# Kernel optimization log

Measured on AMD Instinct MI355X. Metric: run time of the kernel, lower is better.

The kernel has to match this reference:

```python
import jax, jax.numpy as jnp
import numpy as np

B, N, D = 4, 2048, 1024
THRESHOLD_FACTOR = 1.25


def setup_inputs() -> dict:
    key = jax.random.key(0)
    ks = jax.random.split(key, 8)
    s = 0.02  # init scale matching torch.randn * 0.02
    return {
        "hidden_states": jax.random.normal(ks[0], (B, N, D), jnp.float32),
        "Wq": jax.random.normal(ks[1], (D, D), jnp.float32) * s,
        "bq": jnp.zeros((D,), jnp.float32),
        "Wk": jax.random.normal(ks[2], (D, D), jnp.float32) * s,
        "bk": jnp.zeros((D,), jnp.float32),
        "Wv": jax.random.normal(ks[3], (D, D), jnp.float32) * s,
        "bv": jnp.zeros((D,), jnp.float32),
        "Wo": jax.random.normal(ks[4], (D, D), jnp.float32) * s,
        "bo": jnp.zeros((D,), jnp.float32),
        "Wtq": jax.random.normal(ks[5], (2, D), jnp.float32) * s,  # nn.Linear(D, 2)
        "btq": jnp.zeros((2,), jnp.float32),
        "Wfq": jax.random.normal(ks[6], (D, 2), jnp.float32) * s,  # HebbianLinear(2, D)
        "bfq": jnp.zeros((D,), jnp.float32),
    }


def _linear(x, W, b):
    return x @ W.T + b


def reference(hidden_states, Wq, bq, Wk, bk, Wv, bv, Wo, bo, Wtq, btq, Wfq, bfq):
    d = hidden_states.shape[-1]
    q = _linear(hidden_states, Wq, bq)
    k = _linear(hidden_states, Wk, bk)
    v = _linear(hidden_states, Wv, bv)
    scores = jnp.einsum('bid,bjd->bij', q, k) / jnp.sqrt(jnp.asarray(d, scores_dtype := q.dtype))

    # PhaseAwareBinaryAttention on 2-d quantum projection
    qp = _linear(hidden_states, Wtq, btq)            # [B, N, 2]
    diff = qp[:, :, None, :] - qp[:, None, :, :]      # [B, N, N, 2]
    dist_sq = jnp.sum(diff * diff, axis=-1)           # [B, N, N]
    phase_diff = jnp.arctan2(diff[..., 1], diff[..., 0])
    forward_bias = 0.5 * (1.0 + jnp.cos(phase_diff))
    mean_dist = jnp.mean(dist_sq, axis=(-1, -2), keepdims=True)
    std_dist = jnp.std(dist_sq, axis=(-1, -2), keepdims=True, ddof=1)  # torch unbiased std
    threshold = mean_dist + THRESHOLD_FACTOR * std_dist
    n = dist_sq.shape[-1]
    causal = jnp.tril(jnp.ones((n, n), bool))
    valid = (dist_sq <= threshold) & causal[None]
    binary_attn = valid.astype(scores.dtype) * forward_bias

    masked = jnp.where(binary_attn == 0, -jnp.inf, scores)
    weights = jax.nn.softmax(masked, axis=-1)
    context = jnp.einsum('bij,bjd->bid', weights, v)
    output = _linear(context, Wo, bo)

    # F.normalize(qp, p=2, dim=-1) with eps=1e-12
    r_embed = qp / jnp.maximum(jnp.linalg.norm(qp, axis=-1, keepdims=True), 1e-12)
    quantum_output = _linear(r_embed, Wfq, bfq)
    return hidden_states + output + 0.1 * quantum_output
```

## Files before the change

### kernel.cpp

```cpp
#include <hip/hip_runtime.h>
#include <math.h>

#define N_TOK 2048
#define DIM   1024
#define BATCH 4

typedef float v4f  __attribute__((ext_vector_type(4)));
typedef __bf16 v8bf __attribute__((ext_vector_type(8)));
typedef unsigned short v8us __attribute__((ext_vector_type(8)));

static __device__ __forceinline__ unsigned short f2bf(float f) {
  unsigned int u = __float_as_uint(f);
  u += 0x7fffu + ((u >> 16) & 1u);
  return (unsigned short)(u >> 16);
}
static __device__ __forceinline__ float bf2f(unsigned short h) {
  return __uint_as_float((unsigned int)h << 16);
}

__global__ __launch_bounds__(256) void castqp_kernel(
    const float* __restrict__ hs, const float* __restrict__ Wtq,
    const float* __restrict__ btq, unsigned short* __restrict__ hs_b,
    float2* __restrict__ qp, float2* __restrict__ remb) {
  int w = threadIdx.x >> 6, lane = threadIdx.x & 63;
  int row = blockIdx.x * 4 + w;
  const float* x = hs + (size_t)row * DIM;
  unsigned short* d = hs_b + (size_t)row * DIM;
  float a0 = 0.f, a1 = 0.f;
#pragma unroll
  for (int it = 0; it < 4; ++it) {
    int base = it * 256 + lane * 4;
    float4 v = *(const float4*)(x + base);
    float4 w0 = *(const float4*)(Wtq + base);
    float4 w1 = *(const float4*)(Wtq + DIM + base);
    ushort4 pk;
    pk.x = f2bf(v.x); pk.y = f2bf(v.y); pk.z = f2bf(v.z); pk.w = f2bf(v.w);
    *(ushort4*)(d + base) = pk;
    a0 += v.x * w0.x + v.y * w0.y + v.z * w0.z + v.w * w0.w;
    a1 += v.x * w1.x + v.y * w1.y + v.z * w1.z + v.w * w1.w;
  }
  for (int o = 32; o; o >>= 1) { a0 += __shfl_xor(a0, o); a1 += __shfl_xor(a1, o); }
  if (lane == 0) {
    a0 += btq[0]; a1 += btq[1];
    qp[row] = make_float2(a0, a1);
    float nrm = fmaxf(sqrtf(a0 * a0 + a1 * a1), 1e-12f);
    remb[row] = make_float2(a0 / nrm, a1 / nrm);
  }
}

__global__ __launch_bounds__(256) void cast_w4_kernel(
    const float* __restrict__ W0, const float* __restrict__ W1,
    const float* __restrict__ W2, const float* __restrict__ W3,
    unsigned short* __restrict__ D0, unsigned short* __restrict__ D1,
    unsigned short* __restrict__ D2, unsigned short* __restrict__ D3) {
  const float* s;
  unsigned short* d;
  switch (blockIdx.y) {
    case 0: s = W0; d = D0; break;
    case 1: s = W1; d = D1; break;
    case 2: s = W2; d = D2; break;
    default: s = W3; d = D3; break;
  }
  int i = (blockIdx.x * 256 + threadIdx.x) * 4;
  float4 v = *(const float4*)(s + i);
  d[i + 0] = f2bf(v.x); d[i + 1] = f2bf(v.y);
  d[i + 2] = f2bf(v.z); d[i + 3] = f2bf(v.w);
}

__global__ __launch_bounds__(256) void moments_kernel(
    const float2* __restrict__ qp, double* __restrict__ part) {
  int b = blockIdx.y;
  int i0 = blockIdx.x * 32;
  const float2* qb = qp + ((size_t)b << 11);
  double s1 = 0.0, s2 = 0.0;
  for (int idx = threadIdx.x; idx < 32 * N_TOK; idx += 256) {
    int i = i0 + (idx >> 11), j = idx & (N_TOK - 1);
    float2 pi = qb[i], pj = qb[j];
    float dx = pi.x - pj.x, dy = pi.y - pj.y;
    float dd = __fadd_rn(__fmul_rn(dx, dx), __fmul_rn(dy, dy));
    s1 += (double)dd;
    s2 += (double)dd * (double)dd;
  }
  int lane = threadIdx.x & 63, w = threadIdx.x >> 6;
  for (int o = 32; o; o >>= 1) { s1 += __shfl_xor(s1, o); s2 += __shfl_xor(s2, o); }
  __shared__ double red[8];
  if (lane == 0) { red[w] = s1; red[4 + w] = s2; }
  __syncthreads();
  if (threadIdx.x == 0) {
    int slot = b * 64 + blockIdx.x;
    part[slot * 2 + 0] = red[0] + red[1] + red[2] + red[3];
    part[slot * 2 + 1] = red[4] + red[5] + red[6] + red[7];
  }
}

__global__ __launch_bounds__(256) void thr_kernel(
    const double* __restrict__ part, float* __restrict__ thr) {
  int b = threadIdx.x >> 6, lane = threadIdx.x & 63;
  double s1 = part[(b * 64 + lane) * 2 + 0];
  double s2 = part[(b * 64 + lane) * 2 + 1];
  for (int o = 32; o; o >>= 1) { s1 += __shfl_xor(s1, o); s2 += __shfl_xor(s2, o); }
  if (lane == 0) {
    double n2 = (double)N_TOK * (double)N_TOK;
    double mean = s1 / n2;
    double var = (s2 - n2 * mean * mean) / (n2 - 1.0);
    if (var < 0.0) var = 0.0;
    thr[b] = (float)(mean + 1.25 * sqrt(var));
  }
}

__device__ __forceinline__ void gemm_ktile_loop(
    const unsigned short* __restrict__ Ag, const unsigned short* __restrict__ Bg,
    int ldA, int ldB, int kBeg, int kEnd,
    unsigned short* As, unsigned short* Bs, v4f acc[4][4]) {
  const int tid  = threadIdx.x;
  const int lane = tid & 63;
  const int wm   = ((tid >> 6) & 1) << 6, wn = (tid >> 7) << 6;
  const int quad = lane >> 4, l16 = lane & 15;
  const int srow = tid >> 3;
  const int scol = (tid & 7) * 8;
  for (int k0 = kBeg; k0 < kEnd; k0 += 64) {
    __syncthreads();
#pragma unroll
    for (int it = 0; it < 4; ++it) {
      int row = srow + it * 32;
      const unsigned short* ga = Ag + (size_t)row * ldA + k0 + scol;
      const unsigned short* gb = Bg + (size_t)row * ldB + k0 + scol;
      unsigned short* la = As + (size_t)(it * 256 + (tid & ~63)) * 8;
      unsigned short* lb = Bs + (size_t)(it * 256 + (tid & ~63)) * 8;
      __builtin_amdgcn_global_load_lds((const __attribute__((address_space(1))) void*)ga,
                                       (__attribute__((address_space(3))) void*)la, 16, 0, 0);
      __builtin_amdgcn_global_load_lds((const __attribute__((address_space(1))) void*)gb,
                                       (__attribute__((address_space(3))) void*)lb, 16, 0, 0);
    }
    asm volatile("s_waitcnt vmcnt(0)" ::: "memory");
    __syncthreads();
#pragma unroll
    for (int kk = 0; kk < 64; kk += 32) {
      v8bf af[4], bfv[4];
#pragma unroll
      for (int i = 0; i < 4; ++i)
        af[i] = *(const v8bf*)(As + (wm + i * 16 + l16) * 64 + kk + quad * 8);
#pragma unroll
      for (int i = 0; i < 4; ++i)
        bfv[i] = *(const v8bf*)(Bs + (wn + i * 16 + l16) * 64 + kk + quad * 8);
#pragma unroll
      for (int mi = 0; mi < 4; ++mi)
#pragma unroll
        for (int ni = 0; ni < 4; ++ni)
          acc[mi][ni] = __builtin_amdgcn_mfma_f32_16x16x32_bf16(af[mi], bfv[ni], acc[mi][ni], 0, 0, 0);
    }
  }
}

__device__ __forceinline__ void ktile64_loop(
    const unsigned short* __restrict__ Ag, const unsigned short* __restrict__ Bg,
    int ldA, int ldB, int kBeg, int kEnd,
    unsigned short* As, unsigned short* Bs, v4f acc[2][4]) {
  const int tid  = threadIdx.x;
  const int lane = tid & 63;
  const int wr   = ((tid >> 6) & 1) << 5, wc = (tid >> 7) << 6;
  const int quad = lane >> 4, l16 = lane & 15;
  const int srow = tid >> 3;
  const int scol = (tid & 7) * 8;
  for (int k0 = kBeg; k0 < kEnd; k0 += 64) {
    __syncthreads();
#pragma unroll
    for (int it = 0; it < 2; ++it) {
      const unsigned short* ga = Ag + (size_t)(srow + it * 32) * ldA + k0 + scol;
      unsigned short* la = As + (size_t)(it * 256 + (tid & ~63)) * 8;
      __builtin_amdgcn_global_load_lds((const __attribute__((address_space(1))) void*)ga,
                                       (__attribute__((address_space(3))) void*)la, 16, 0, 0);
    }
#pragma unroll
    for (int it = 0; it < 4; ++it) {
      const unsigned short* gb = Bg + (size_t)(srow + it * 32) * ldB + k0 + scol;
      unsigned short* lb = Bs + (size_t)(it * 256 + (tid & ~63)) * 8;
      __builtin_amdgcn_global_load_lds((const __attribute__((address_space(1))) void*)gb,
                                       (__attribute__((address_space(3))) void*)lb, 16, 0, 0);
    }
    asm volatile("s_waitcnt vmcnt(0)" ::: "memory");
    __syncthreads();
#pragma unroll
    for (int kk = 0; kk < 64; kk += 32) {
      v8bf af[2], bfv[4];
#pragma unroll
      for (int i = 0; i < 2; ++i)
        af[i] = *(const v8bf*)(As + (wr + i * 16 + l16) * 64 + kk + quad * 8);
#pragma unroll
      for (int i = 0; i < 4; ++i)
        bfv[i] = *(const v8bf*)(Bs + (wc + i * 16 + l16) * 64 + kk + quad * 8);
#pragma unroll
      for (int mi = 0; mi < 2; ++mi)
#pragma unroll
        for (int ni = 0; ni < 4; ++ni)
          acc[mi][ni] = __builtin_amdgcn_mfma_f32_16x16x32_bf16(af[mi], bfv[ni], acc[mi][ni], 0, 0, 0);
    }
  }
}

#define PROLOG128                                                     \
  __shared__ __attribute__((aligned(16))) unsigned short smem[2][128 * 64];\
  unsigned short* As = smem[0];                                       \
  unsigned short* Bs = smem[1];                                       \
  v4f acc[4][4];                                                      \
  _Pragma("unroll") for (int i_ = 0; i_ < 4; ++i_)                    \
  _Pragma("unroll") for (int j_ = 0; j_ < 4; ++j_)                    \
      acc[i_][j_] = v4f{0.f, 0.f, 0.f, 0.f};                          \
  const int lane = threadIdx.x & 63, w = threadIdx.x >> 6;            \
  const int wm = (w & 1) << 6, wn = (w >> 1) << 6;                    \
  const int quad = lane >> 4, l16 = lane & 15;

#define PROLOG64                                                      \
  __shared__ __attribute__((aligned(16))) unsigned short As[64 * 64]; \
  __shared__ __attribute__((aligned(16))) unsigned short Bs[128 * 64];\
  v4f acc[2][4];                                                      \
  _Pragma("unroll") for (int i_ = 0; i_ < 2; ++i_)                    \
  _Pragma("unroll") for (int j_ = 0; j_ < 4; ++j_)                    \
      acc[i_][j_] = v4f{0.f, 0.f, 0.f, 0.f};                          \
  const int lane = threadIdx.x & 63, w = threadIdx.x >> 6;            \
  const int wr = (w & 1) << 5, wc = (w >> 1) << 6;                    \
  const int quad = lane >> 4, l16 = lane & 15;

__global__ __launch_bounds__(256) void gemm_qkv_fused_kernel(
    const unsigned short* __restrict__ X, const unsigned short* __restrict__ Wqkv,
    const float* __restrict__ bq, const float* __restrict__ bk,
    const float* __restrict__ bv, unsigned short* __restrict__ q_b,
    unsigned short* __restrict__ k_b, unsigned short* __restrict__ v_t) {
  PROLOG128
  int m0 = blockIdx.y * 128, n0 = blockIdx.x * 128;
  gemm_ktile_loop(X + (size_t)m0 * DIM, Wqkv + (size_t)n0 * DIM, DIM, DIM, 0, DIM, As, Bs, acc);
  int region = n0 >> 10;
  const float* bias = region == 0 ? bq : region == 1 ? bk : bv;
  int cbase = n0 & 1023;
  if (region < 2) {
    unsigned short* dst = region == 0 ? q_b : k_b;
#pragma unroll
    for (int mi = 0; mi < 4; ++mi) {
      int row0 = m0 + wm + mi * 16 + quad * 4;
#pragma unroll
      for (int ni = 0; ni < 4; ++ni) {
        int col = cbase + wn + ni * 16 + l16;
        float bcol = bias[col];
#pragma unroll
        for (int r = 0; r < 4; ++r)
          dst[(size_t)(row0 + r) * DIM + col] = f2bf(acc[mi][ni][r] + bcol);
      }
    }
  } else {
    unsigned short* T = &smem[0][0];
    __syncthreads();
#pragma unroll
    for (int mi = 0; mi < 4; ++mi) {
      int trow = wm + mi * 16 + quad * 4;
#pragma unroll
      for (int ni = 0; ni < 4; ++ni) {
        int fcol = wn + ni * 16 + l16;
        float bcol = bias[cbase + fcol];
        ushort4 pk;
        pk.x = f2bf(acc[mi][ni][0] + bcol);
        pk.y = f2bf(acc[mi][ni][1] + bcol);
        pk.z = f2bf(acc[mi][ni][2] + bcol);
        pk.w = f2bf(acc[mi][ni][3] + bcol);
        *(ushort4*)(T + fcol * 128 + trow) = pk;
      }
    }
    __syncthreads();
    int bb = m0 >> 11, tok0 = m0 & (N_TOK - 1);
    unsigned short* dstb = v_t + ((size_t)(bb << 10) + cbase) * N_TOK + tok0;
#pragma unroll
    for (int kk2 = 0; kk2 < 8; ++kk2) {
      int c = kk2 * 256 + threadIdx.x;
      int f = c >> 4, e0 = (c & 15) * 8;
      v8us v = *(const v8us*)(T + f * 128 + e0);
      *(v8us*)(dstb + (size_t)f * N_TOK + e0) = v;
    }
  }
}

static __device__ __forceinline__ int tri_cum(int T) {
  int m = T >> 1;
  return (T & 1) ? (m + 1) * (m + 1) : m * (m + 1);
}
__global__ __launch_bounds__(256) void gemm_scores_kernel(
    const unsigned short* __restrict__ q, const unsigned short* __restrict__ k,
    const float2* __restrict__ qp, const float* __restrict__ thr,
    unsigned short* __restrict__ S) {
  PROLOG64
  int b = blockIdx.y;
  int t = blockIdx.x;
  int ti = 2 * (int)sqrtf((float)t);
  if (ti > 31) ti = 31;
  while (ti < 31 && tri_cum(ti + 1) <= t) ++ti;
  while (tri_cum(ti) > t) --ti;
  int tj = t - tri_cum(ti);
  int i0 = ti * 64, j0 = tj * 128;
  const unsigned short* qb = q + (size_t)b * N_TOK * DIM;
  const unsigned short* kb = k + (size_t)b * N_TOK * DIM;
  ktile64_loop(qb + (size_t)i0 * DIM, kb + (size_t)j0 * DIM, DIM, DIM, 0, DIM, As, Bs, acc);
  float th = thr[b];
  const float2* qpb = qp + ((size_t)b << 11);
  unsigned short* Sb = S + (size_t)b * N_TOK * N_TOK;
  float2 pjv[4];
#pragma unroll
  for (int ni = 0; ni < 4; ++ni) pjv[ni] = qpb[j0 + wc + ni * 16 + l16];
#pragma unroll
  for (int mi = 0; mi < 2; ++mi) {
#pragma unroll
    for (int r = 0; r < 4; ++r) {
      int i = i0 + wr + mi * 16 + quad * 4 + r;
      float2 pi2 = qpb[i];
#pragma unroll
      for (int ni = 0; ni < 4; ++ni) {
        int j = j0 + wc + ni * 16 + l16;
        if (j <= i) {
          float dx = pi2.x - pjv[ni].x, dy = pi2.y - pjv[ni].y;
          float dd = __fadd_rn(__fmul_rn(dx, dx), __fmul_rn(dy, dy));
          bool ok = (dd <= th);
          if (ok && dx < 0.f && fabsf(dy) <= 3e-4f * (-dx)) {
            float fb = 0.5f * (1.f + cosf(atan2f(dy, dx)));
            if (fb == 0.f) ok = false;
          }
          Sb[(size_t)i * N_TOK + j] = ok ? f2bf(acc[mi][ni][r] * 0.03125f) : 0xFF80;
        }
      }
    }
  }
}

__global__ __launch_bounds__(256) void softmax_kernel(
    const unsigned short* __restrict__ S, unsigned short* __restrict__ P) {
  int row = blockIdx.x;
  int b = row >> 11, i = row & (N_TOK - 1);
  const unsigned short* s = S + ((size_t)b * N_TOK + i) * N_TOK;
  unsigned short* p = P + ((size_t)b * N_TOK + i) * N_TOK;
  int tid = threadIdx.x, lane = tid & 63, w = tid >> 6;
  int lim = i + 1;
  int tail0 = lim & ~7, ntail = lim - tail0;
  __shared__ float redmax[4], redsum[4];
  float mx = -__builtin_inff();
  for (int j = tid * 8; j + 8 <= lim; j += 2048) {
    v8us v = *(const v8us*)(s + j);
#pragma unroll
    for (int e = 0; e < 8; ++e) mx = fmaxf(mx, bf2f(v[e]));
  }
  if (tid < ntail) mx = fmaxf(mx, bf2f(s[tail0 + tid]));
  for (int o = 32; o; o >>= 1) mx = fmaxf(mx, __shfl_xor(mx, o));
  if (lane == 0) redmax[w] = mx;
  __syncthreads();
  mx = fmaxf(fmaxf(redmax[0], redmax[1]), fmaxf(redmax[2], redmax[3]));
  float sum = 0.f;
  for (int j = tid * 8; j + 8 <= lim; j += 2048) {
    v8us v = *(const v8us*)(s + j);
#pragma unroll
    for (int e = 0; e < 8; ++e) sum += __expf(bf2f(v[e]) - mx);
  }
  if (tid < ntail) sum += __expf(bf2f(s[tail0 + tid]) - mx);
  for (int o = 32; o; o >>= 1) sum += __shfl_xor(sum, o);
  if (lane == 0) redsum[w] = sum;
  __syncthreads();
  sum = redsum[0] + redsum[1] + redsum[2] + redsum[3];
  float inv = 1.f / sum;
  for (int j = tid * 8; j + 8 <= lim; j += 2048) {
    v8us v = *(const v8us*)(s + j);
    v8us o;
#pragma unroll
    for (int e = 0; e < 8; ++e) o[e] = f2bf(__expf(bf2f(v[e]) - mx) * inv);
    *(v8us*)(p + j) = o;
  }
  if (tid < ntail) p[tail0 + tid] = f2bf(__expf(bf2f(s[tail0 + tid]) - mx) * inv);
  int zs = (lim + 7) & ~7;
  if (tid < zs - lim) p[lim + tid] = 0;
  v8us zv;
#pragma unroll
  for (int e = 0; e < 8; ++e) zv[e] = 0;
  for (int j = zs + tid * 8; j < N_TOK; j += 2048) *(v8us*)(p + j) = zv;
}

__global__ __launch_bounds__(256) void gemm_pv_kernel(
    const unsigned short* __restrict__ P, const unsigned short* __restrict__ vt,
    unsigned short* __restrict__ ctx) {
  PROLOG64
  int b = blockIdx.z;
  int ti = blockIdx.y, d0 = blockIdx.x * 128;
  int i0 = ti * 64;
  const unsigned short* Pb = P + (size_t)b * N_TOK * N_TOK;
  const unsigned short* Vb = vt + (size_t)b * DIM * N_TOK;
  int kEnd = ((ti + 2) >> 1) * 128;
  ktile64_loop(Pb + (size_t)i0 * N_TOK, Vb + (size_t)d0 * N_TOK, N_TOK, N_TOK, 0, kEnd, As, Bs, acc);
#pragma unroll
  for (int mi = 0; mi < 2; ++mi) {
    int row0 = i0 + wr + mi * 16 + quad * 4;
#pragma unroll
    for (int ni = 0; ni < 4; ++ni) {
      int d = d0 + wc + ni * 16 + l16;
#pragma unroll
      for (int r = 0; r < 4; ++r)
        ctx[((size_t)b * N_TOK + row0 + r) * DIM + d] = f2bf(acc[mi][ni][r]);
    }
  }
}

__global__ __launch_bounds__(256) void gemm_out_kernel(
    const unsigned short* __restrict__ ctx, const unsigned short* __restrict__ Wob,
    const float* __restrict__ bo, const float* __restrict__ hs,
    const float2* __restrict__ remb, const float* __restrict__ Wfq,
    const float* __restrict__ bfq, float* __restrict__ out) {
  PROLOG64
  int m0 = blockIdx.y * 64, n0 = blockIdx.x * 128;
  ktile64_loop(ctx + (size_t)m0 * DIM, Wob + (size_t)n0 * DIM, DIM, DIM, 0, DIM, As, Bs, acc);
#pragma unroll
  for (int mi = 0; mi < 2; ++mi) {
    int row0 = m0 + wr + mi * 16 + quad * 4;
#pragma unroll
    for (int ni = 0; ni < 4; ++ni) {
      int col = n0 + wc + ni * 16 + l16;
      float bias2 = bo[col] + 0.1f * bfq[col];
      float wf0 = 0.1f * Wfq[col * 2 + 0], wf1 = 0.1f * Wfq[col * 2 + 1];
#pragma unroll
      for (int r = 0; r < 4; ++r) {
        int row = row0 + r;
        float2 re = remb[row];
        out[(size_t)row * DIM + col] =
            acc[mi][ni][r] + bias2 + hs[(size_t)row * DIM + col] + re.x * wf0 + re.y * wf1;
      }
    }
  }
}

extern "C" void kernel_launch(void* const* d_in, const int* in_sizes, int n_in,
                              void* d_out, int out_size, void* d_ws, size_t ws_size,
                              hipStream_t stream) {
  const float* hs  = (const float*)d_in[0];
  const float* Wq  = (const float*)d_in[1];
  const float* bq  = (const float*)d_in[2];
  const float* Wk  = (const float*)d_in[3];
  const float* bk  = (const float*)d_in[4];
  const float* Wv  = (const float*)d_in[5];
  const float* bv  = (const float*)d_in[6];
  const float* Wo  = (const float*)d_in[7];
  const float* bo  = (const float*)d_in[8];
  const float* Wtq = (const float*)d_in[9];
  const float* btq = (const float*)d_in[10];
  const float* Wfq = (const float*)d_in[11];
  const float* bfq = (const float*)d_in[12];
  float* out = (float*)d_out;

  char* ws = (char*)d_ws;
  size_t off = 0;
  auto alloc = [&](size_t bytes) {
    char* p = ws + off;
    off += (bytes + 255) & ~(size_t)255;
    return p;
  };
  unsigned short* hs_b = (unsigned short*)alloc((size_t)8192 * 1024 * 2);
  unsigned short* q_b  = (unsigned short*)alloc((size_t)8192 * 1024 * 2);
  unsigned short* k_b  = (unsigned short*)alloc((size_t)8192 * 1024 * 2);
  unsigned short* v_t  = (unsigned short*)alloc((size_t)8192 * 1024 * 2);
  unsigned short* Wq_b = (unsigned short*)alloc((size_t)1024 * 1024 * 2);
  unsigned short* Wk_b = (unsigned short*)alloc((size_t)1024 * 1024 * 2);
  unsigned short* Wv_b = (unsigned short*)alloc((size_t)1024 * 1024 * 2);
  unsigned short* Wo_b = (unsigned short*)alloc((size_t)1024 * 1024 * 2);
  float2* qp   = (float2*)alloc((size_t)8192 * 8);
  float2* remb = (float2*)alloc((size_t)8192 * 8);
  double* part = (double*)alloc((size_t)BATCH * 64 * 2 * 8);
  float*  thr  = (float*)alloc(64);
  unsigned short* S = (unsigned short*)alloc((size_t)BATCH * N_TOK * N_TOK * 2);
  unsigned short* P   = q_b;
  unsigned short* ctx = hs_b;

  castqp_kernel<<<2048, 256, 0, stream>>>(hs, Wtq, btq, hs_b, qp, remb);
  cast_w4_kernel<<<dim3(1024, 4), 256, 0, stream>>>(Wq, Wk, Wv, Wo, Wq_b, Wk_b, Wv_b, Wo_b);
  moments_kernel<<<dim3(64, BATCH), 256, 0, stream>>>((const float2*)qp, part);
  thr_kernel<<<1, 256, 0, stream>>>(part, thr);

  gemm_qkv_fused_kernel<<<dim3(24, 64), 256, 0, stream>>>(
      hs_b, Wq_b, bq, bk, bv, q_b, k_b, v_t);

  gemm_scores_kernel<<<dim3(272, 4), 256, 0, stream>>>(
      q_b, k_b, (const float2*)qp, thr, S);

  softmax_kernel<<<8192, 256, 0, stream>>>(S, P);

  gemm_pv_kernel<<<dim3(8, 32, 4), 256, 0, stream>>>(P, v_t, ctx);

  gemm_out_kernel<<<dim3(8, 128), 256, 0, stream>>>(ctx, Wo_b, bo, hs, remb, Wfq, bfq, out);
}
```

Baseline: 395.7 us.

## Fuse softmax normalization into PV GEMM A-tile load and remap blocks per XCD

```diff
diff --git a/kernel.cpp b/kernel.cpp
--- a/kernel.cpp
+++ b/kernel.cpp
@@ -227,7 +227,11 @@
     const float* __restrict__ bv, unsigned short* __restrict__ q_b,
     unsigned short* __restrict__ k_b, unsigned short* __restrict__ v_t) {
   PROLOG128
-  int m0 = blockIdx.y * 128, n0 = blockIdx.x * 128;
+  int lid = blockIdx.y * 24 + blockIdx.x;
+  int xcd = lid & 7, slot = lid >> 3;
+  int by = (xcd << 3) | (slot & 7);
+  int bx = slot >> 3;
+  int m0 = by * 128, n0 = bx * 128;
   gemm_ktile_loop(X + (size_t)m0 * DIM, Wqkv + (size_t)n0 * DIM, DIM, DIM, 0, DIM, As, Bs, acc);
   int region = n0 >> 10;
   const float* bias = region == 0 ? bq : region == 1 ? bk : bv;
@@ -327,66 +331,97 @@
   }
 }
 
-__global__ __launch_bounds__(256) void softmax_kernel(
-    const unsigned short* __restrict__ S, unsigned short* __restrict__ P) {
-  int row = blockIdx.x;
+__global__ __launch_bounds__(256) void stats_kernel(
+    const unsigned short* __restrict__ S, float2* __restrict__ stats) {
+  int w = threadIdx.x >> 6, lane = threadIdx.x & 63;
+  int row = blockIdx.x * 4 + w;
   int b = row >> 11, i = row & (N_TOK - 1);
   const unsigned short* s = S + ((size_t)b * N_TOK + i) * N_TOK;
-  unsigned short* p = P + ((size_t)b * N_TOK + i) * N_TOK;
-  int tid = threadIdx.x, lane = tid & 63, w = tid >> 6;
   int lim = i + 1;
-  int tail0 = lim & ~7, ntail = lim - tail0;
-  __shared__ float redmax[4], redsum[4];
   float mx = -__builtin_inff();
-  for (int j = tid * 8; j + 8 <= lim; j += 2048) {
-    v8us v = *(const v8us*)(s + j);
-#pragma unroll
-    for (int e = 0; e < 8; ++e) mx = fmaxf(mx, bf2f(v[e]));
-  }
-  if (tid < ntail) mx = fmaxf(mx, bf2f(s[tail0 + tid]));
+  for (int j = lane * 8; j < lim; j += 512) {
+    if (j + 8 <= lim) {
+      v8us v = *(const v8us*)(s + j);
+#pragma unroll
+      for (int e = 0; e < 8; ++e) mx = fmaxf(mx, bf2f(v[e]));
+    } else {
+      for (int e = 0; e < lim - j; ++e) mx = fmaxf(mx, bf2f(s[j + e]));
+    }
+  }
   for (int o = 32; o; o >>= 1) mx = fmaxf(mx, __shfl_xor(mx, o));
-  if (lane == 0) redmax[w] = mx;
-  __syncthreads();
-  mx = fmaxf(fmaxf(redmax[0], redmax[1]), fmaxf(redmax[2], redmax[3]));
   float sum = 0.f;
-  for (int j = tid * 8; j + 8 <= lim; j += 2048) {
-    v8us v = *(const v8us*)(s + j);
-#pragma unroll
-    for (int e = 0; e < 8; ++e) sum += __expf(bf2f(v[e]) - mx);
-  }
-  if (tid < ntail) sum += __expf(bf2f(s[tail0 + tid]) - mx);
+  for (int j = lane * 8; j < lim; j += 512) {
+    if (j + 8 <= lim) {
+      v8us v = *(const v8us*)(s + j);
+#pragma unroll
+      for (int e = 0; e < 8; ++e) sum += __expf(bf2f(v[e]) - mx);
+    } else {
+      for (int e = 0; e < lim - j; ++e) sum += __expf(bf2f(s[j + e]) - mx);
+    }
+  }
   for (int o = 32; o; o >>= 1) sum += __shfl_xor(sum, o);
-  if (lane == 0) redsum[w] = sum;
-  __syncthreads();
-  sum = redsum[0] + redsum[1] + redsum[2] + redsum[3];
-  float inv = 1.f / sum;
-  for (int j = tid * 8; j + 8 <= lim; j += 2048) {
-    v8us v = *(const v8us*)(s + j);
-    v8us o;
-#pragma unroll
-    for (int e = 0; e < 8; ++e) o[e] = f2bf(__expf(bf2f(v[e]) - mx) * inv);
-    *(v8us*)(p + j) = o;
-  }
-  if (tid < ntail) p[tail0 + tid] = f2bf(__expf(bf2f(s[tail0 + tid]) - mx) * inv);
-  int zs = (lim + 7) & ~7;
-  if (tid < zs - lim) p[lim + tid] = 0;
-  v8us zv;
-#pragma unroll
-  for (int e = 0; e < 8; ++e) zv[e] = 0;
-  for (int j = zs + tid * 8; j < N_TOK; j += 2048) *(v8us*)(p + j) = zv;
+  if (lane == 0) stats[row] = make_float2(mx, 1.f / sum);
 }
 
 __global__ __launch_bounds__(256) void gemm_pv_kernel(
-    const unsigned short* __restrict__ P, const unsigned short* __restrict__ vt,
-    unsigned short* __restrict__ ctx) {
-  PROLOG64
-  int b = blockIdx.z;
-  int ti = blockIdx.y, d0 = blockIdx.x * 128;
-  int i0 = ti * 64;
-  const unsigned short* Pb = P + (size_t)b * N_TOK * N_TOK;
-  const unsigned short* Vb = vt + (size_t)b * DIM * N_TOK;
+    const unsigned short* __restrict__ S, const float2* __restrict__ stats,
+    const unsigned short* __restrict__ vt, unsigned short* __restrict__ ctx) {
+  __shared__ __attribute__((aligned(16))) unsigned short As[64 * 64];
+  __shared__ __attribute__((aligned(16))) unsigned short Bs[128 * 64];
+  v4f acc[2][4];
+#pragma unroll
+  for (int i_ = 0; i_ < 2; ++i_)
+#pragma unroll
+    for (int j_ = 0; j_ < 4; ++j_) acc[i_][j_] = v4f{0.f, 0.f, 0.f, 0.f};
+  const int tid = threadIdx.x, lane = tid & 63, w = tid >> 6;
+  const int wr = (w & 1) << 5, wc = (w >> 1) << 6;
+  const int quad = lane >> 4, l16 = lane & 15;
+  const int srow = tid >> 3, scol = (tid & 7) * 8;
+  int b = blockIdx.z, ti = blockIdx.y, d0 = blockIdx.x * 128, i0 = ti * 64;
+  const unsigned short* Sb = S + (size_t)b * N_TOK * N_TOK;
+  const unsigned short* Vb = vt + ((size_t)b * DIM + d0) * N_TOK;
+  const float2* stb = stats + ((size_t)b << 11);
+  float2 st[2] = {stb[i0 + srow], stb[i0 + srow + 32]};
   int kEnd = ((ti + 2) >> 1) * 128;
-  ktile64_loop(Pb + (size_t)i0 * N_TOK, Vb + (size_t)d0 * N_TOK, N_TOK, N_TOK, 0, kEnd, As, Bs, acc);
+  for (int k0 = 0; k0 < kEnd; k0 += 64) {
+    __syncthreads();
+#pragma unroll
+    for (int it = 0; it < 2; ++it) {
+      int r = srow + it * 32, gi = i0 + r, gj = k0 + scol;
+      v8us sv = *(const v8us*)(Sb + (size_t)gi * N_TOK + gj);
+      v8us pk8;
+#pragma unroll
+      for (int e = 0; e < 8; ++e)
+        pk8[e] = (gj + e <= gi)
+                     ? f2bf(__expf(bf2f(sv[e]) - st[it].x) * st[it].y)
+                     : (unsigned short)0;
+      *(v8us*)(As + r * 64 + scol) = pk8;
+    }
+#pragma unroll
+    for (int it = 0; it < 4; ++it) {
+      const unsigned short* gb = Vb + (size_t)(srow + it * 32) * N_TOK + k0 + scol;
+      unsigned short* lb = Bs + (size_t)(it * 256 + (tid & ~63)) * 8;
+      __builtin_amdgcn_global_load_lds((const __attribute__((address_space(1))) void*)gb,
+                                       (__attribute__((address_space(3))) void*)lb, 16, 0, 0);
+    }
+    asm volatile("s_waitcnt vmcnt(0)" ::: "memory");
+    __syncthreads();
+#pragma unroll
+    for (int kk = 0; kk < 64; kk += 32) {
+      v8bf af[2], bfv[4];
+#pragma unroll
+      for (int i = 0; i < 2; ++i)
+        af[i] = *(const v8bf*)(As + (wr + i * 16 + l16) * 64 + kk + quad * 8);
+#pragma unroll
+      for (int i = 0; i < 4; ++i)
+        bfv[i] = *(const v8bf*)(Bs + (wc + i * 16 + l16) * 64 + kk + quad * 8);
+#pragma unroll
+      for (int mi = 0; mi < 2; ++mi)
+#pragma unroll
+        for (int ni = 0; ni < 4; ++ni)
+          acc[mi][ni] = __builtin_amdgcn_mfma_f32_16x16x32_bf16(af[mi], bfv[ni], acc[mi][ni], 0, 0, 0);
+    }
+  }
 #pragma unroll
   for (int mi = 0; mi < 2; ++mi) {
     int row0 = i0 + wr + mi * 16 + quad * 4;
@@ -406,7 +441,11 @@
     const float2* __restrict__ remb, const float* __restrict__ Wfq,
     const float* __restrict__ bfq, float* __restrict__ out) {
   PROLOG64
-  int m0 = blockIdx.y * 64, n0 = blockIdx.x * 128;
+  int lid = blockIdx.y * 8 + blockIdx.x;
+  int xcd = lid & 7, slot = lid >> 3;
+  int by = (xcd << 4) | (slot & 15);
+  int bx = slot >> 4;
+  int m0 = by * 64, n0 = bx * 128;
   ktile64_loop(ctx + (size_t)m0 * DIM, Wob + (size_t)n0 * DIM, DIM, DIM, 0, DIM, As, Bs, acc);
 #pragma unroll
   for (int mi = 0; mi < 2; ++mi) {
@@ -460,12 +499,12 @@
   unsigned short* Wk_b = (unsigned short*)alloc((size_t)1024 * 1024 * 2);
   unsigned short* Wv_b = (unsigned short*)alloc((size_t)1024 * 1024 * 2);
   unsigned short* Wo_b = (unsigned short*)alloc((size_t)1024 * 1024 * 2);
-  float2* qp   = (float2*)alloc((size_t)8192 * 8);
-  float2* remb = (float2*)alloc((size_t)8192 * 8);
-  double* part = (double*)alloc((size_t)BATCH * 64 * 2 * 8);
-  float*  thr  = (float*)alloc(64);
+  float2* qp    = (float2*)alloc((size_t)8192 * 8);
+  float2* remb  = (float2*)alloc((size_t)8192 * 8);
+  float2* stats = (float2*)alloc((size_t)8192 * 8);
+  double* part  = (double*)alloc((size_t)BATCH * 64 * 2 * 8);
+  float*  thr   = (float*)alloc(64);
   unsigned short* S = (unsigned short*)alloc((size_t)BATCH * N_TOK * N_TOK * 2);
-  unsigned short* P   = q_b;
   unsigned short* ctx = hs_b;
 
   castqp_kernel<<<2048, 256, 0, stream>>>(hs, Wtq, btq, hs_b, qp, remb);
@@ -479,9 +518,9 @@
   gemm_scores_kernel<<<dim3(272, 4), 256, 0, stream>>>(
       q_b, k_b, (const float2*)qp, thr, S);
 
-  softmax_kernel<<<8192, 256, 0, stream>>>(S, P);
-
-  gemm_pv_kernel<<<dim3(8, 32, 4), 256, 0, stream>>>(P, v_t, ctx);
+  stats_kernel<<<2048, 256, 0, stream>>>(S, stats);
+
+  gemm_pv_kernel<<<dim3(8, 32, 4), 256, 0, stream>>>(S, (const float2*)stats, v_t, ctx);
 
   gemm_out_kernel<<<dim3(8, 128), 256, 0, stream>>>(ctx, Wo_b, bo, hs, remb, Wfq, bfq, out);
 }
```

New measurement: 412.9 us. 4.3% more time.

## Shrink attention GEMM tiles to 64x64 and add XCD-aware block swizzles

Applied to the files above, without the earlier changes.

```diff
diff --git a/kernel.cpp b/kernel.cpp
--- a/kernel.cpp
+++ b/kernel.cpp
@@ -152,17 +152,17 @@
   }
 }
 
-__device__ __forceinline__ void ktile64_loop(
+__device__ __forceinline__ void ktile6464_loop(
     const unsigned short* __restrict__ Ag, const unsigned short* __restrict__ Bg,
-    int ldA, int ldB, int kBeg, int kEnd,
-    unsigned short* As, unsigned short* Bs, v4f acc[2][4]) {
+    int ldA, int ldB, int kEnd,
+    unsigned short* As, unsigned short* Bs, v4f acc[2][2]) {
   const int tid  = threadIdx.x;
   const int lane = tid & 63;
-  const int wr   = ((tid >> 6) & 1) << 5, wc = (tid >> 7) << 6;
+  const int wr   = ((tid >> 6) & 1) << 5, wc = (tid >> 7) << 5;
   const int quad = lane >> 4, l16 = lane & 15;
   const int srow = tid >> 3;
   const int scol = (tid & 7) * 8;
-  for (int k0 = kBeg; k0 < kEnd; k0 += 64) {
+  for (int k0 = 0; k0 < kEnd; k0 += 64) {
     __syncthreads();
 #pragma unroll
     for (int it = 0; it < 2; ++it) {
@@ -172,7 +172,7 @@
                                        (__attribute__((address_space(3))) void*)la, 16, 0, 0);
     }
 #pragma unroll
-    for (int it = 0; it < 4; ++it) {
+    for (int it = 0; it < 2; ++it) {
       const unsigned short* gb = Bg + (size_t)(srow + it * 32) * ldB + k0 + scol;
       unsigned short* lb = Bs + (size_t)(it * 256 + (tid & ~63)) * 8;
       __builtin_amdgcn_global_load_lds((const __attribute__((address_space(1))) void*)gb,
@@ -182,17 +182,17 @@
     __syncthreads();
 #pragma unroll
     for (int kk = 0; kk < 64; kk += 32) {
-      v8bf af[2], bfv[4];
+      v8bf af[2], bfv[2];
 #pragma unroll
       for (int i = 0; i < 2; ++i)
         af[i] = *(const v8bf*)(As + (wr + i * 16 + l16) * 64 + kk + quad * 8);
 #pragma unroll
-      for (int i = 0; i < 4; ++i)
+      for (int i = 0; i < 2; ++i)
         bfv[i] = *(const v8bf*)(Bs + (wc + i * 16 + l16) * 64 + kk + quad * 8);
 #pragma unroll
       for (int mi = 0; mi < 2; ++mi)
 #pragma unroll
-        for (int ni = 0; ni < 4; ++ni)
+        for (int ni = 0; ni < 2; ++ni)
           acc[mi][ni] = __builtin_amdgcn_mfma_f32_16x16x32_bf16(af[mi], bfv[ni], acc[mi][ni], 0, 0, 0);
     }
   }
@@ -210,15 +210,15 @@
   const int wm = (w & 1) << 6, wn = (w >> 1) << 6;                    \
   const int quad = lane >> 4, l16 = lane & 15;
 
-#define PROLOG64                                                      \
+#define PROLOG6464                                                    \
   __shared__ __attribute__((aligned(16))) unsigned short As[64 * 64]; \
-  __shared__ __attribute__((aligned(16))) unsigned short Bs[128 * 64];\
-  v4f acc[2][4];                                                      \
+  __shared__ __attribute__((aligned(16))) unsigned short Bs[64 * 64]; \
+  v4f acc[2][2];                                                      \
   _Pragma("unroll") for (int i_ = 0; i_ < 2; ++i_)                    \
-  _Pragma("unroll") for (int j_ = 0; j_ < 4; ++j_)                    \
+  _Pragma("unroll") for (int j_ = 0; j_ < 2; ++j_)                    \
       acc[i_][j_] = v4f{0.f, 0.f, 0.f, 0.f};                          \
   const int lane = threadIdx.x & 63, w = threadIdx.x >> 6;            \
-  const int wr = (w & 1) << 5, wc = (w >> 1) << 6;                    \
+  const int wr = (w & 1) << 5, wc = (w >> 1) << 5;                    \
   const int quad = lane >> 4, l16 = lane & 15;
 
 __global__ __launch_bounds__(256) void gemm_qkv_fused_kernel(
@@ -227,7 +227,11 @@
     const float* __restrict__ bv, unsigned short* __restrict__ q_b,
     unsigned short* __restrict__ k_b, unsigned short* __restrict__ v_t) {
   PROLOG128
-  int m0 = blockIdx.y * 128, n0 = blockIdx.x * 128;
+  int lid = blockIdx.y * 24 + blockIdx.x;
+  int xcd = lid & 7, slot = lid >> 3;
+  int by = (xcd << 3) | (slot & 7);
+  int bx = slot >> 3;
+  int m0 = by * 128, n0 = bx * 128;
   gemm_ktile_loop(X + (size_t)m0 * DIM, Wqkv + (size_t)n0 * DIM, DIM, DIM, 0, DIM, As, Bs, acc);
   int region = n0 >> 10;
   const float* bias = region == 0 ? bq : region == 1 ? bk : bv;
@@ -277,32 +281,28 @@
   }
 }
 
-static __device__ __forceinline__ int tri_cum(int T) {
-  int m = T >> 1;
-  return (T & 1) ? (m + 1) * (m + 1) : m * (m + 1);
-}
 __global__ __launch_bounds__(256) void gemm_scores_kernel(
     const unsigned short* __restrict__ q, const unsigned short* __restrict__ k,
     const float2* __restrict__ qp, const float* __restrict__ thr,
     unsigned short* __restrict__ S) {
-  PROLOG64
+  PROLOG6464
   int b = blockIdx.y;
-  int t = blockIdx.x;
-  int ti = 2 * (int)sqrtf((float)t);
-  if (ti > 31) ti = 31;
-  while (ti < 31 && tri_cum(ti + 1) <= t) ++ti;
-  while (tri_cum(ti) > t) --ti;
-  int tj = t - tri_cum(ti);
-  int i0 = ti * 64, j0 = tj * 128;
+  int bx = blockIdx.x;
+  int t = (bx & 7) * 66 + (bx >> 3);
+  int ti = (int)((sqrtf(8.f * (float)t + 1.f) - 1.f) * 0.5f);
+  while ((ti + 1) * (ti + 2) / 2 <= t) ++ti;
+  while (ti * (ti + 1) / 2 > t) --ti;
+  int tj = t - ti * (ti + 1) / 2;
+  int i0 = ti * 64, j0 = tj * 64;
   const unsigned short* qb = q + (size_t)b * N_TOK * DIM;
   const unsigned short* kb = k + (size_t)b * N_TOK * DIM;
-  ktile64_loop(qb + (size_t)i0 * DIM, kb + (size_t)j0 * DIM, DIM, DIM, 0, DIM, As, Bs, acc);
+  ktile6464_loop(qb + (size_t)i0 * DIM, kb + (size_t)j0 * DIM, DIM, DIM, DIM, As, Bs, acc);
   float th = thr[b];
   const float2* qpb = qp + ((size_t)b << 11);
   unsigned short* Sb = S + (size_t)b * N_TOK * N_TOK;
-  float2 pjv[4];
-#pragma unroll
-  for (int ni = 0; ni < 4; ++ni) pjv[ni] = qpb[j0 + wc + ni * 16 + l16];
+  float2 pjv[2];
+#pragma unroll
+  for (int ni = 0; ni < 2; ++ni) pjv[ni] = qpb[j0 + wc + ni * 16 + l16];
 #pragma unroll
   for (int mi = 0; mi < 2; ++mi) {
 #pragma unroll
@@ -310,7 +310,7 @@
       int i = i0 + wr + mi * 16 + quad * 4 + r;
       float2 pi2 = qpb[i];
 #pragma unroll
-      for (int ni = 0; ni < 4; ++ni) {
+      for (int ni = 0; ni < 2; ++ni) {
         int j = j0 + wc + ni * 16 + l16;
         if (j <= i) {
           float dx = pi2.x - pjv[ni].x, dy = pi2.y - pjv[ni].y;
@@ -379,19 +379,19 @@
 __global__ __launch_bounds__(256) void gemm_pv_kernel(
     const unsigned short* __restrict__ P, const unsigned short* __restrict__ vt,
     unsigned short* __restrict__ ctx) {
-  PROLOG64
+  PROLOG6464
   int b = blockIdx.z;
-  int ti = blockIdx.y, d0 = blockIdx.x * 128;
+  int ti = blockIdx.y, d0 = blockIdx.x * 64;
   int i0 = ti * 64;
   const unsigned short* Pb = P + (size_t)b * N_TOK * N_TOK;
-  const unsigned short* Vb = vt + (size_t)b * DIM * N_TOK;
-  int kEnd = ((ti + 2) >> 1) * 128;
-  ktile64_loop(Pb + (size_t)i0 * N_TOK, Vb + (size_t)d0 * N_TOK, N_TOK, N_TOK, 0, kEnd, As, Bs, acc);
+  const unsigned short* Vb = vt + ((size_t)b * DIM + d0) * N_TOK;
+  int kEnd = (ti + 1) * 64;
+  ktile6464_loop(Pb + (size_t)i0 * N_TOK, Vb, N_TOK, N_TOK, kEnd, As, Bs, acc);
 #pragma unroll
   for (int mi = 0; mi < 2; ++mi) {
     int row0 = i0 + wr + mi * 16 + quad * 4;
 #pragma unroll
-    for (int ni = 0; ni < 4; ++ni) {
+    for (int ni = 0; ni < 2; ++ni) {
       int d = d0 + wc + ni * 16 + l16;
 #pragma unroll
       for (int r = 0; r < 4; ++r)
@@ -405,14 +405,18 @@
     const float* __restrict__ bo, const float* __restrict__ hs,
     const float2* __restrict__ remb, const float* __restrict__ Wfq,
     const float* __restrict__ bfq, float* __restrict__ out) {
-  PROLOG64
-  int m0 = blockIdx.y * 64, n0 = blockIdx.x * 128;
-  ktile64_loop(ctx + (size_t)m0 * DIM, Wob + (size_t)n0 * DIM, DIM, DIM, 0, DIM, As, Bs, acc);
+  PROLOG6464
+  int lid = blockIdx.y * 16 + blockIdx.x;
+  int xcd = lid & 7, slot = lid >> 3;
+  int by = (xcd << 4) | (slot & 15);
+  int bx = slot >> 4;
+  int m0 = by * 64, n0 = bx * 64;
+  ktile6464_loop(ctx + (size_t)m0 * DIM, Wob + (size_t)n0 * DIM, DIM, DIM, DIM, As, Bs, acc);
 #pragma unroll
   for (int mi = 0; mi < 2; ++mi) {
     int row0 = m0 + wr + mi * 16 + quad * 4;
 #pragma unroll
-    for (int ni = 0; ni < 4; ++ni) {
+    for (int ni = 0; ni < 2; ++ni) {
       int col = n0 + wc + ni * 16 + l16;
       float bias2 = bo[col] + 0.1f * bfq[col];
       float wf0 = 0.1f * Wfq[col * 2 + 0], wf1 = 0.1f * Wfq[col * 2 + 1];
@@ -476,12 +480,12 @@
   gemm_qkv_fused_kernel<<<dim3(24, 64), 256, 0, stream>>>(
       hs_b, Wq_b, bq, bk, bv, q_b, k_b, v_t);
 
-  gemm_scores_kernel<<<dim3(272, 4), 256, 0, stream>>>(
+  gemm_scores_kernel<<<dim3(528, 4), 256, 0, stream>>>(
       q_b, k_b, (const float2*)qp, thr, S);
 
   softmax_kernel<<<8192, 256, 0, stream>>>(S, P);
 
-  gemm_pv_kernel<<<dim3(8, 32, 4), 256, 0, stream>>>(P, v_t, ctx);
-
-  gemm_out_kernel<<<dim3(8, 128), 256, 0, stream>>>(ctx, Wo_b, bo, hs, remb, Wfq, bfq, out);
-}
+  gemm_pv_kernel<<<dim3(16, 32, 4), 256, 0, stream>>>(P, v_t, ctx);
+
+  gemm_out_kernel<<<dim3(16, 128), 256, 0, stream>>>(ctx, Wo_b, bo, hs, remb, Wfq, bfq, out);
+}
```

Result: faster. 378.5 us (-4.3%).
